# Optimization experiments

Hardware: AMD Instinct MI355X
Metric: run time of the kernel (lower is better)

Reference implementation:

```python
import jax, jax.numpy as jnp
import numpy as np

N, L, S, H, D = 2, 4096, 4096, 8, 32


def setup_inputs() -> dict:
    key = jax.random.key(0)
    kq, kk, kv, km = jax.random.split(key, 4)
    queries = jax.random.normal(kq, (N, L, H, D), dtype=jnp.float32)
    keys = jax.random.normal(kk, (N, S, H, D), dtype=jnp.float32)
    values = jax.random.normal(kv, (N, S, H, D), dtype=jnp.float32)
    q_mask = jnp.ones((N, L), dtype=bool)
    kv_mask = jax.random.randint(km, (N, S), 0, 2).astype(bool)
    return {"queries": queries, "keys": keys, "values": values,
            "q_mask": q_mask, "kv_mask": kv_mask}


def reference(queries, keys, values, q_mask, kv_mask):
    # QK: [N, L, S, H] -- contraction over head dim D (GEMM form of the
    # original broadcast-multiply-sum).
    QK = jnp.einsum('nlhd,nshd->nlsh', queries, keys)
    mask = q_mask[:, :, None] & kv_mask[:, None, :]            # [N, L, S]
    QK = jnp.where(mask[..., None], QK, -jnp.inf)
    softmax_temp = 1.0 / np.sqrt(D).astype(np.float32)
    A = jax.nn.softmax(softmax_temp * QK, axis=2)              # softmax over S
    # weighted value sum: [N, L, H, D]
    return jnp.einsum('nlsh,nshd->nlhd', A, values)
```

## Files before the change

### kernel.cpp

```cpp
#include <hip/hip_runtime.h>
#include <stdint.h>
#include <math.h>


typedef __bf16 bf16x8 __attribute__((ext_vector_type(8)));
typedef float  f32x16 __attribute__((ext_vector_type(16)));
typedef float  f32x4  __attribute__((ext_vector_type(4)));

#define C2 0.25502407414058425f

#define BUF_OFF_B 64

__global__ __launch_bounds__(256) void prep(
    const float* __restrict__ K, const float* __restrict__ V,
    const int* __restrict__ KM, int* __restrict__ W, __bf16* __restrict__ BUF)
{
    const int wib = threadIdx.x >> 6, lane = threadIdx.x & 63;
    const int n = blockIdx.x >> 8;
    __shared__ int csum[64];
    __shared__ int idx[4096];

    const int* m = KM + n * 4096;
    for (int c = wib; c < 64; c += 4) {
        unsigned long long bal = __ballot(m[c * 64 + lane] != 0);
        if (lane == 0) csum[c] = __popcll(bal);
    }
    __syncthreads();
    if (wib == 0) {
        int v = csum[lane];
        #pragma unroll
        for (int off = 1; off < 64; off <<= 1) {
            int u = __shfl_up(v, off);
            if (lane >= off) v += u;
        }
        csum[lane] = v;
    }
    __syncthreads();
    const int total = csum[63];
    for (int c = wib; c < 64; c += 4) {
        bool mm = m[c * 64 + lane] != 0;
        unsigned long long bal = __ballot(mm);
        int base = c ? csum[c - 1] : 0;
        int pre = __popcll(bal & ((1ull << lane) - 1ull));
        if (mm) idx[base + pre] = c * 64 + lane;
    }
    const int cnt32 = (total + 31) & ~31;
    for (int j = total + (int)threadIdx.x; j < cnt32; j += 256) idx[j] = 0;
    __syncthreads();

    if (threadIdx.x == 0 && (blockIdx.x & 255) == 0) W[n] = total;

    const int gt = blockIdx.x * 4 + wib;
    const int h = (gt >> 7) & 7, t = gt & 127;
    if (t >= ((total + 31) >> 5)) return;
    const int hi = lane >> 5, lq = lane & 31;
    const float* Kb = K + (size_t)n * 4096 * 256 + h * 32;
    const float* Vb = V + (size_t)n * 4096 * 256 + h * 32;
    __bf16* dst = BUF + (size_t)gt * 2048 + lane * 8;

    const float* krow = Kb + (size_t)idx[t * 32 + lq] * 256 + 8 * hi;
    #pragma unroll
    for (int f = 0; f < 2; ++f) {
        f32x4 a = *(const f32x4*)(krow + 16 * f);
        f32x4 b = *(const f32x4*)(krow + 16 * f + 4);
        bf16x8 o8;
        o8[0] = (__bf16)a[0]; o8[1] = (__bf16)a[1]; o8[2] = (__bf16)a[2]; o8[3] = (__bf16)a[3];
        o8[4] = (__bf16)b[0]; o8[5] = (__bf16)b[1]; o8[6] = (__bf16)b[2]; o8[7] = (__bf16)b[3];
        *(bf16x8*)(dst + f * 512) = o8;
    }
    #pragma unroll
    for (int f = 0; f < 2; ++f) {
        bf16x8 o8;
        #pragma unroll
        for (int j = 0; j < 8; ++j) {
            int s = t * 32 + 16 * f + (j & 3) + 4 * hi + 8 * ((j >> 2) & 1);
            o8[j] = (__bf16)Vb[(size_t)idx[s] * 256 + lq];
        }
        *(bf16x8*)(dst + 1024 + f * 512) = o8;
    }
}

__global__ __launch_bounds__(256, 4) void fattn32(
    const float* __restrict__ Q, const __bf16* __restrict__ BUF,
    const int* __restrict__ W, float* __restrict__ Out)
{
    const int tid  = threadIdx.x;
    const int lane = tid & 63;
    const int wib  = tid >> 6;
    const int b  = blockIdx.x;
    const int w  = (b & 7) * 64 + (b >> 3);
    const int qg = w & 31;
    const int h  = (w >> 5) & 7;
    const int n  = w >> 8;
    const int qt = qg * 4 + wib;
    const int hi = lane >> 5;
    const int lq = lane & 31;

    const int cnt    = W[n];
    const int ntiles = (cnt + 31) >> 5;

    const float* qrow = Q + ((size_t)n * 4096 + qt * 32 + lq) * 256 + h * 32 + 8 * hi;
    bf16x8 qf0, qf1;
    {
        f32x4 a0 = *(const f32x4*)(qrow);
        f32x4 b0 = *(const f32x4*)(qrow + 4);
        f32x4 a1 = *(const f32x4*)(qrow + 16);
        f32x4 b1 = *(const f32x4*)(qrow + 20);
        #pragma unroll
        for (int j = 0; j < 4; ++j) {
            qf0[j]     = (__bf16)(C2 * a0[j]);
            qf0[4 + j] = (__bf16)(C2 * b0[j]);
            qf1[j]     = (__bf16)(C2 * a1[j]);
            qf1[4 + j] = (__bf16)(C2 * b1[j]);
        }
    }

    __shared__ float pool[4352];
    uint8_t* sb = (uint8_t*)pool;

    const uint8_t* bufbase = (const uint8_t*)BUF + (size_t)((n * 8 + h) * 128) * 4096;
    const uint8_t* ssrc = bufbase + tid * 16;

    f32x16 o = {};
    float l = 0.0f;
    const f32x16 z = {};

    uint4 stg = *(const uint4*)(ssrc);

    for (int t = 0; t < ntiles; ++t) {
        *(uint4*)(sb + (t & 1) * 4096 + tid * 16) = stg;
        if (t + 1 < ntiles)
            stg = *(const uint4*)(ssrc + (size_t)(t + 1) * 4096);
        asm volatile("s_waitcnt lgkmcnt(0)\n\ts_barrier" ::: "memory");

        const __bf16* tb = (const __bf16*)(sb + (t & 1) * 4096) + lane * 8;
        bf16x8 kf0 = *(const bf16x8*)(tb);
        bf16x8 kf1 = *(const bf16x8*)(tb + 512);
        bf16x8 vf0 = *(const bf16x8*)(tb + 1024);
        bf16x8 vf1 = *(const bf16x8*)(tb + 1536);

        f32x16 st = __builtin_amdgcn_mfma_f32_32x32x16_bf16(kf0, qf0, z, 0, 0, 0);
        st = __builtin_amdgcn_mfma_f32_32x32x16_bf16(kf1, qf1, st, 0, 0, 0);

        float p[16];
        #pragma unroll
        for (int r = 0; r < 16; ++r)
            p[r] = __builtin_amdgcn_exp2f(st[r]);

        const int kb = t * 32;
        if (kb + 32 > cnt) {
            #pragma unroll
            for (int r = 0; r < 16; ++r) {
                int ks = kb + (r & 3) + 8 * ((r >> 2) & 1) + 16 * (r >> 3) + 4 * hi;
                if (ks >= cnt) p[r] = 0.0f;
            }
        }

        l += (((p[0] + p[1]) + (p[2] + p[3])) + ((p[4] + p[5]) + (p[6] + p[7])))
           + (((p[8] + p[9]) + (p[10] + p[11])) + ((p[12] + p[13]) + (p[14] + p[15])));

        bf16x8 pf0, pf1;
        #pragma unroll
        for (int j = 0; j < 8; ++j) { pf0[j] = (__bf16)p[j]; pf1[j] = (__bf16)p[8 + j]; }

        o = __builtin_amdgcn_mfma_f32_32x32x16_bf16(vf0, pf0, o, 0, 0, 0);
        o = __builtin_amdgcn_mfma_f32_32x32x16_bf16(vf1, pf1, o, 0, 0, 0);
    }

    float lt  = l + __shfl_xor(l, 32);
    float inv = 1.0f / lt;
    __syncthreads();
    float* tp = pool + wib * 1056;
    #pragma unroll
    for (int r = 0; r < 16; ++r) {
        int d = (r & 3) + 8 * (r >> 2) + 4 * hi;
        tp[lq * 33 + d] = o[r] * inv;
    }
    asm volatile("s_waitcnt lgkmcnt(0)" ::: "memory");

    const int qr = lane >> 1;
    const int dh = (lane & 1) * 16;
    float* orow = Out + (((size_t)(n * 4096 + qt * 32 + qr)) * 8 + h) * 32 + dh;
    #pragma unroll
    for (int k2 = 0; k2 < 4; ++k2) {
        f32x4 vst;
        vst[0] = tp[qr * 33 + dh + 4 * k2 + 0];
        vst[1] = tp[qr * 33 + dh + 4 * k2 + 1];
        vst[2] = tp[qr * 33 + dh + 4 * k2 + 2];
        vst[3] = tp[qr * 33 + dh + 4 * k2 + 3];
        *(f32x4*)(orow + 4 * k2) = vst;
    }
}

extern "C" void kernel_launch(void* const* d_in, const int* in_sizes, int n_in,
                              void* d_out, int out_size, void* d_ws, size_t ws_size,
                              hipStream_t stream) {
    const float* Q = (const float*)d_in[0];
    const float* K = (const float*)d_in[1];
    const float* V = (const float*)d_in[2];
    const int* KM = (const int*)d_in[4];
    float* Out = (float*)d_out;

    int* Wk = (int*)d_ws;
    __bf16* BUF = (__bf16*)((char*)d_ws + BUF_OFF_B);

    hipLaunchKernelGGL(prep,    dim3(512), dim3(256), 0, stream, K, V, KM, Wk, BUF);
    hipLaunchKernelGGL(fattn32, dim3(512), dim3(256), 0, stream, Q, BUF, Wk, Out);
}
```

Baseline: 46.49 us.

## Split KV tiles across waves with two query tiles per wave and LDS reduction

Each block now handles two 32-row query tiles for one head. Its four waves split the key/value tiles among themselves instead of each wave looping over all tiles, and each wave reuses every loaded K/V fragment for both query tiles. The per-tile LDS staging and block barrier are gone; K/V fragments are read straight from global memory. Partial outputs and row sums are combined through shared memory at the end. The grid doubles, in exchange for more LDS, an extra reduction pass, and the unnormalized softmax still not subtracting the max.

```diff
diff --git a/kernel.cpp b/kernel.cpp
--- a/kernel.cpp
+++ b/kernel.cpp
@@ -88,107 +88,130 @@
     const int lane = tid & 63;
     const int wib  = tid >> 6;
     const int b  = blockIdx.x;
-    const int w  = (b & 7) * 64 + (b >> 3);
-    const int qg = w & 31;
-    const int h  = (w >> 5) & 7;
-    const int n  = w >> 8;
-    const int qt = qg * 4 + wib;
+    const int w  = (b & 7) * 128 + (b >> 3);
+    const int qp = w & 63;
+    const int h  = (w >> 6) & 7;
+    const int n  = w >> 9;
     const int hi = lane >> 5;
     const int lq = lane & 31;
 
     const int cnt    = W[n];
     const int ntiles = (cnt + 31) >> 5;
-
-    const float* qrow = Q + ((size_t)n * 4096 + qt * 32 + lq) * 256 + h * 32 + 8 * hi;
-    bf16x8 qf0, qf1;
+    const int qt0 = qp * 2, qt1 = qp * 2 + 1;
+
+    bf16x8 qa0, qa1, qb0, qb1;
     {
-        f32x4 a0 = *(const f32x4*)(qrow);
-        f32x4 b0 = *(const f32x4*)(qrow + 4);
-        f32x4 a1 = *(const f32x4*)(qrow + 16);
-        f32x4 b1 = *(const f32x4*)(qrow + 20);
-        #pragma unroll
-        for (int j = 0; j < 4; ++j) {
-            qf0[j]     = (__bf16)(C2 * a0[j]);
-            qf0[4 + j] = (__bf16)(C2 * b0[j]);
-            qf1[j]     = (__bf16)(C2 * a1[j]);
-            qf1[4 + j] = (__bf16)(C2 * b1[j]);
-        }
-    }
-
-    __shared__ float pool[4352];
-    uint8_t* sb = (uint8_t*)pool;
-
-    const uint8_t* bufbase = (const uint8_t*)BUF + (size_t)((n * 8 + h) * 128) * 4096;
-    const uint8_t* ssrc = bufbase + tid * 16;
-
-    f32x16 o = {};
-    float l = 0.0f;
+        const float* qr0 = Q + ((size_t)n * 4096 + qt0 * 32 + lq) * 256 + h * 32 + 8 * hi;
+        const float* qr1 = qr0 + 32 * 256;
+        f32x4 a, bb;
+        a = *(const f32x4*)(qr0);      bb = *(const f32x4*)(qr0 + 4);
+        #pragma unroll
+        for (int j = 0; j < 4; ++j) { qa0[j] = (__bf16)(C2 * a[j]); qa0[4 + j] = (__bf16)(C2 * bb[j]); }
+        a = *(const f32x4*)(qr0 + 16); bb = *(const f32x4*)(qr0 + 20);
+        #pragma unroll
+        for (int j = 0; j < 4; ++j) { qa1[j] = (__bf16)(C2 * a[j]); qa1[4 + j] = (__bf16)(C2 * bb[j]); }
+        a = *(const f32x4*)(qr1);      bb = *(const f32x4*)(qr1 + 4);
+        #pragma unroll
+        for (int j = 0; j < 4; ++j) { qb0[j] = (__bf16)(C2 * a[j]); qb0[4 + j] = (__bf16)(C2 * bb[j]); }
+        a = *(const f32x4*)(qr1 + 16); bb = *(const f32x4*)(qr1 + 20);
+        #pragma unroll
+        for (int j = 0; j < 4; ++j) { qb1[j] = (__bf16)(C2 * a[j]); qb1[4 + j] = (__bf16)(C2 * bb[j]); }
+    }
+
+    const __bf16* bufp = BUF + (size_t)((n * 8 + h) * 128) * 2048 + lane * 8;
+
+    f32x16 oa = {}, ob = {};
+    float la = 0.0f, lb = 0.0f;
     const f32x16 z = {};
 
-    uint4 stg = *(const uint4*)(ssrc);
-
-    for (int t = 0; t < ntiles; ++t) {
-        *(uint4*)(sb + (t & 1) * 4096 + tid * 16) = stg;
-        if (t + 1 < ntiles)
-            stg = *(const uint4*)(ssrc + (size_t)(t + 1) * 4096);
-        asm volatile("s_waitcnt lgkmcnt(0)\n\ts_barrier" ::: "memory");
-
-        const __bf16* tb = (const __bf16*)(sb + (t & 1) * 4096) + lane * 8;
+    for (int t = wib; t < ntiles; t += 4) {
+        const __bf16* tb = bufp + (size_t)t * 2048;
         bf16x8 kf0 = *(const bf16x8*)(tb);
         bf16x8 kf1 = *(const bf16x8*)(tb + 512);
         bf16x8 vf0 = *(const bf16x8*)(tb + 1024);
         bf16x8 vf1 = *(const bf16x8*)(tb + 1536);
 
-        f32x16 st = __builtin_amdgcn_mfma_f32_32x32x16_bf16(kf0, qf0, z, 0, 0, 0);
-        st = __builtin_amdgcn_mfma_f32_32x32x16_bf16(kf1, qf1, st, 0, 0, 0);
-
-        float p[16];
-        #pragma unroll
-        for (int r = 0; r < 16; ++r)
-            p[r] = __builtin_amdgcn_exp2f(st[r]);
-
         const int kb = t * 32;
-        if (kb + 32 > cnt) {
-            #pragma unroll
-            for (int r = 0; r < 16; ++r) {
-                int ks = kb + (r & 3) + 8 * ((r >> 2) & 1) + 16 * (r >> 3) + 4 * hi;
-                if (ks >= cnt) p[r] = 0.0f;
+        const bool tail = (kb + 32 > cnt);
+
+        {
+            f32x16 st = __builtin_amdgcn_mfma_f32_32x32x16_bf16(kf0, qa0, z, 0, 0, 0);
+            st = __builtin_amdgcn_mfma_f32_32x32x16_bf16(kf1, qa1, st, 0, 0, 0);
+            float p[16];
+            #pragma unroll
+            for (int r = 0; r < 16; ++r)
+                p[r] = __builtin_amdgcn_exp2f(st[r]);
+            if (tail) {
+                #pragma unroll
+                for (int r = 0; r < 16; ++r) {
+                    int ks = kb + (r & 3) + 8 * ((r >> 2) & 1) + 16 * (r >> 3) + 4 * hi;
+                    if (ks >= cnt) p[r] = 0.0f;
+                }
             }
-        }
-
-        l += (((p[0] + p[1]) + (p[2] + p[3])) + ((p[4] + p[5]) + (p[6] + p[7])))
-           + (((p[8] + p[9]) + (p[10] + p[11])) + ((p[12] + p[13]) + (p[14] + p[15])));
-
-        bf16x8 pf0, pf1;
-        #pragma unroll
-        for (int j = 0; j < 8; ++j) { pf0[j] = (__bf16)p[j]; pf1[j] = (__bf16)p[8 + j]; }
-
-        o = __builtin_amdgcn_mfma_f32_32x32x16_bf16(vf0, pf0, o, 0, 0, 0);
-        o = __builtin_amdgcn_mfma_f32_32x32x16_bf16(vf1, pf1, o, 0, 0, 0);
-    }
-
-    float lt  = l + __shfl_xor(l, 32);
-    float inv = 1.0f / lt;
-    __syncthreads();
-    float* tp = pool + wib * 1056;
+            la += (((p[0] + p[1]) + (p[2] + p[3])) + ((p[4] + p[5]) + (p[6] + p[7])))
+                + (((p[8] + p[9]) + (p[10] + p[11])) + ((p[12] + p[13]) + (p[14] + p[15])));
+            bf16x8 pf0, pf1;
+            #pragma unroll
+            for (int j = 0; j < 8; ++j) { pf0[j] = (__bf16)p[j]; pf1[j] = (__bf16)p[8 + j]; }
+            oa = __builtin_amdgcn_mfma_f32_32x32x16_bf16(vf0, pf0, oa, 0, 0, 0);
+            oa = __builtin_amdgcn_mfma_f32_32x32x16_bf16(vf1, pf1, oa, 0, 0, 0);
+        }
+        {
+            f32x16 st = __builtin_amdgcn_mfma_f32_32x32x16_bf16(kf0, qb0, z, 0, 0, 0);
+            st = __builtin_amdgcn_mfma_f32_32x32x16_bf16(kf1, qb1, st, 0, 0, 0);
+            float p[16];
+            #pragma unroll
+            for (int r = 0; r < 16; ++r)
+                p[r] = __builtin_amdgcn_exp2f(st[r]);
+            if (tail) {
+                #pragma unroll
+                for (int r = 0; r < 16; ++r) {
+                    int ks = kb + (r & 3) + 8 * ((r >> 2) & 1) + 16 * (r >> 3) + 4 * hi;
+                    if (ks >= cnt) p[r] = 0.0f;
+                }
+            }
+            lb += (((p[0] + p[1]) + (p[2] + p[3])) + ((p[4] + p[5]) + (p[6] + p[7])))
+                + (((p[8] + p[9]) + (p[10] + p[11])) + ((p[12] + p[13]) + (p[14] + p[15])));
+            bf16x8 pf0, pf1;
+            #pragma unroll
+            for (int j = 0; j < 8; ++j) { pf0[j] = (__bf16)p[j]; pf1[j] = (__bf16)p[8 + j]; }
+            ob = __builtin_amdgcn_mfma_f32_32x32x16_bf16(vf0, pf0, ob, 0, 0, 0);
+            ob = __builtin_amdgcn_mfma_f32_32x32x16_bf16(vf1, pf1, ob, 0, 0, 0);
+        }
+    }
+
+    __shared__ float xt[8][32 * 33];
+    __shared__ float Ls[8][32];
+
+    float lta = la + __shfl_xor(la, 32);
+    float ltb = lb + __shfl_xor(lb, 32);
     #pragma unroll
     for (int r = 0; r < 16; ++r) {
         int d = (r & 3) + 8 * (r >> 2) + 4 * hi;
-        tp[lq * 33 + d] = o[r] * inv;
-    }
-    asm volatile("s_waitcnt lgkmcnt(0)" ::: "memory");
-
-    const int qr = lane >> 1;
-    const int dh = (lane & 1) * 16;
-    float* orow = Out + (((size_t)(n * 4096 + qt * 32 + qr)) * 8 + h) * 32 + dh;
-    #pragma unroll
-    for (int k2 = 0; k2 < 4; ++k2) {
-        f32x4 vst;
-        vst[0] = tp[qr * 33 + dh + 4 * k2 + 0];
-        vst[1] = tp[qr * 33 + dh + 4 * k2 + 1];
-        vst[2] = tp[qr * 33 + dh + 4 * k2 + 2];
-        vst[3] = tp[qr * 33 + dh + 4 * k2 + 3];
-        *(f32x4*)(orow + 4 * k2) = vst;
+        xt[wib][lq * 33 + d]     = oa[r];
+        xt[4 + wib][lq * 33 + d] = ob[r];
+    }
+    if (hi == 0) { Ls[wib][lq] = lta; Ls[4 + wib][lq] = ltb; }
+    __syncthreads();
+
+    const int q  = tid >> 3;
+    const int dg = (tid & 7) * 4;
+    #pragma unroll
+    for (int half = 0; half < 2; ++half) {
+        float ltot = Ls[4 * half + 0][q] + Ls[4 * half + 1][q]
+                   + Ls[4 * half + 2][q] + Ls[4 * half + 3][q];
+        float inv = 1.0f / ltot;
+        f32x4 acc = {};
+        #pragma unroll
+        for (int wv = 0; wv < 4; ++wv) {
+            #pragma unroll
+            for (int jj = 0; jj < 4; ++jj)
+                acc[jj] += xt[4 * half + wv][q * 33 + dg + jj];
+        }
+        acc[0] *= inv; acc[1] *= inv; acc[2] *= inv; acc[3] *= inv;
+        const int qt = (half == 0) ? qt0 : qt1;
+        float* orow = Out + (((size_t)(n * 4096 + qt * 32 + q)) * 8 + h) * 32 + dg;
+        *(f32x4*)orow = acc;
     }
 }
 
@@ -204,6 +227,6 @@
     int* Wk = (int*)d_ws;
     __bf16* BUF = (__bf16*)((char*)d_ws + BUF_OFF_B);
 
-    hipLaunchKernelGGL(prep,    dim3(512), dim3(256), 0, stream, K, V, KM, Wk, BUF);
-    hipLaunchKernelGGL(fattn32, dim3(512), dim3(256), 0, stream, Q, BUF, Wk, Out);
+    hipLaunchKernelGGL(prep,    dim3(512),  dim3(256), 0, stream, K, V, KM, Wk, BUF);
+    hipLaunchKernelGGL(fattn32, dim3(1024), dim3(256), 0, stream, Q, BUF, Wk, Out);
 }
```

Measured after the change: 44.33 us. 4.7% less time.
